# Optimization experiments

Hardware: AMD Instinct MI355X
Metric: run time of the kernel (lower is better)

The kernel has to match this reference:

```python
import jax, jax.numpy as jnp
import numpy as np

N_SAMPLES = 32768
DAMPING = 0.9998
EPS = 1e-8


def sim(home, tensions, masses, gains, mics, forces, home_modifier):
    # forces, home_modifier: (B, M, D, T); home: (1,1,D,1)
    B, M, D, T = forces.shape
    h = home + home_modifier                          # (B,M,D,T)
    f_t = jnp.moveaxis(forces, -1, 0)                 # (T,B,M,D)
    h_t = jnp.moveaxis(h, -1, 0)                      # (T,B,M,D)

    def step(carry, xs):
        pos, vel = carry
        f, hh = xs
        direction = hh - pos
        acc = f + tensions * direction / masses
        vel = (vel + acc) * DAMPING
        pos = pos + vel
        # mic readout: tanh(vel*gains) dotted with mics over dim
        r = jnp.sum(jnp.tanh(vel * gains) * mics, axis=-1)  # (B,M)
        return (pos, vel), (r, direction)

    init = (jnp.zeros((B, M, D), forces.dtype), jnp.zeros((B, M, D), forces.dtype))
    _, (rec, disp) = jax.lax.scan(step, init, (f_t, h_t))
    recording = jnp.moveaxis(rec, 0, -1)              # (B,M,T)
    displacement = jnp.moveaxis(disp, 0, -1)          # (B,M,D,T)
    return recording, displacement


def interpolate_last_axis(x, size):
    # linear interpolation along last axis (F.interpolate mode='linear', align_corners=False)
    T = x.shape[-1]
    pos = jnp.clip((jnp.arange(size) + 0.5) * (T / size) - 0.5, 0.0, T - 1)
    i0 = jnp.floor(pos).astype(jnp.int32)
    i1 = jnp.minimum(i0 + 1, T - 1)
    w = (pos - i0).astype(x.dtype)
    return x[..., i0] * (1 - w) + x[..., i1] * w


def fft_resample(x, desired):
    # zero-pad spectrum to upsample
    spec = jnp.fft.rfft(x, axis=-1, norm='ortho')
    n_coeffs = desired // 2 + 1
    new = jnp.zeros(x.shape[:-1] + (n_coeffs,), dtype=spec.dtype)
    new = new.at[..., :spec.shape[-1]].set(spec)
    return jnp.fft.irfft(new, n=desired, axis=-1, norm='ortho')


def fft_convolve(a, b):
    # linear convolution via 2N-padded FFT, truncated to N
    n = a.shape[-1]
    pa = jnp.pad(a, [(0, 0)] * (a.ndim - 1) + [(0, n)])
    pb = jnp.pad(b, [(0, 0)] * (b.ndim - 1) + [(0, b.shape[-1])])
    spec = jnp.fft.rfft(pa, axis=-1) * jnp.fft.rfft(pb, axis=-1)
    return jnp.fft.irfft(spec, axis=-1)[..., :n]


def forward(forces, home_modifier, filters, home, masses, tensions, gains, mics, to_filter_mixture):
    recording, displacement = sim(home, tensions, masses, gains, mics, forces, home_modifier)
    mixture = jnp.einsum('bmdt,df->bmft', displacement, to_filter_mixture)
    mixture = interpolate_last_axis(mixture, N_SAMPLES)               # (B,M,F,S)
    upsampled = fft_resample(recording, N_SAMPLES)                    # (B,M,S)
    noise = jax.random.uniform(jax.random.key(1), upsampled.shape,
                               dtype=upsampled.dtype, minval=-1.0, maxval=1.0)
    upsampled = jnp.abs(upsampled) * noise
    f = jnp.pad(filters, ((0, 0), (0, 0), (0, N_SAMPLES - filters.shape[-1])))[:, None, :, :]  # (B,1,F,S)
    f = f / (jnp.linalg.norm(f, axis=-1, keepdims=True) + EPS)
    filtered = fft_convolve(f, upsampled[:, :, None, :])              # (B,M,F,S)
    hf = jnp.einsum('bmfs,bmfs->bms', mixture, filtered) + upsampled  # (B,M,S)
    return recording, displacement, hf


def setup_inputs():
    key = jax.random.key(0)
    ks = jax.random.split(key, 8)
    B, M, D, T, F_, L = 2, 32, 64, 2048, 16, 512
    return {
        'forces': jax.random.normal(ks[0], (B, M, D, T), jnp.float32) * 0.01,
        'home_modifier': jax.random.normal(ks[1], (B, M, D, T), jnp.float32),
        'filters': jax.random.normal(ks[2], (B, F_, L), jnp.float32),
        'home': jnp.zeros((1, 1, D, 1), jnp.float32),
        'masses': jax.random.uniform(ks[3], (1, M, 1), jnp.float32, 1000.0, 10000.0),
        'tensions': jax.random.uniform(ks[4], (1, M, D), jnp.float32, 20.0, 30.0),
        'gains': jax.random.uniform(ks[5], (1, M, 1), jnp.float32, 10.0, 100.0),
        'mics': jax.random.uniform(ks[6], (1, M, D), jnp.float32, -1.0, 1.0),
        'to_filter_mixture': jax.random.uniform(ks[7], (D, F_), jnp.float32, -1.0, 1.0),
    }


def reference(forces, home_modifier, filters, home, masses, tensions, gains, mics, to_filter_mixture):
    return forward(forces, home_modifier, filters, home, masses, tensions, gains, mics, to_filter_mixture)
```

## Files before the change

### kernel.cpp

```cpp
#include <hip/hip_runtime.h>
#include <cstdint>
#include <cstddef>

#define DAMP 0.9998f

typedef __attribute__((ext_vector_type(8))) short bf16x8;
typedef __attribute__((ext_vector_type(4))) unsigned short u16x4;
typedef __attribute__((ext_vector_type(4))) float f32x4;

__device__ __forceinline__ unsigned short f2bf(float x) {
    unsigned u = __float_as_uint(x);
    unsigned r = (u + 0x7FFFu + ((u >> 16) & 1u)) >> 16;
    return (unsigned short)r;
}
__device__ __forceinline__ float bf2f(unsigned short v) {
    return __uint_as_float((unsigned)v << 16);
}

__device__ __forceinline__ void threefry_0j(unsigned j, unsigned& o0, unsigned& o1) {
    unsigned x0 = 0u;
    unsigned x1 = j + 1u;
    const unsigned ks2 = 0x1BD11BDBu;
#define TFR(r) { x0 += x1; x1 = (x1 << (r)) | (x1 >> (32 - (r))); x1 ^= x0; }
    TFR(13) TFR(15) TFR(26) TFR(6)
    x0 += 1u;   x1 += ks2 + 1u;
    TFR(17) TFR(29) TFR(16) TFR(24)
    x0 += ks2;  x1 += 0u + 2u;
    TFR(13) TFR(15) TFR(26) TFR(6)
       x1 += 1u + 3u;
    TFR(17) TFR(29) TFR(16) TFR(24)
    x0 += 1u;   x1 += ks2 + 4u;
    TFR(13) TFR(15) TFR(26) TFR(6)
    x0 += ks2;  x1 += 0u + 5u;
#undef TFR
    o0 = x0; o1 = x1;
}

__device__ __forceinline__ float noise_at(unsigned j) {
    unsigned o0, o1;
    threefry_0j(j, o0, o1);
    unsigned bits = o0 ^ o1;
    float u = __uint_as_float((bits >> 9) | 0x3F800000u) - 1.0f;
    return fmaxf(-1.0f, u * 2.0f - 1.0f);
}

__device__ __forceinline__ float dir_val(unsigned u) {
    if (u == 0u) return 2049.f;
    const float PIO = 9.58737992e-05f;
    unsigned y = (2049u * u) & 65535u;
    float sgn = 1.f;
    if (y >= 32768u) { y -= 32768u; sgn = -1.f; }
    unsigned yy = (y > 16384u) ? (32768u - y) : y;
    float sy = sgn * sinf((float)yy * PIO);
    unsigned uu = (u > 16384u) ? (32768u - u) : u;
    float su = sinf((float)uu * PIO);
    return sy / su;
}

__global__ __launch_bounds__(64) void sim_pass1(const float* __restrict__ forces,
                                                const float* __restrict__ hmod,
                                                const float* __restrict__ home,
                                                const float* __restrict__ masses,
                                                const float* __restrict__ tensions,
                                                float* __restrict__ w,
                                                const float* __restrict__ filters,
                                                unsigned short* __restrict__ dirrev,
                                                unsigned short* __restrict__ fnrev) {
    const int blk = blockIdx.x;
    const int d = threadIdx.x;
    if (blk >= 4608) {
        const int row = blk - 4608;
        const float* src = filters + (size_t)row * 512;
        float s = 0.f;
        for (int i = d; i < 512; i += 64) { const float v = src[i]; s += v * v; }
        #pragma unroll
        for (int off = 32; off; off >>= 1) s += __shfl_xor(s, off);
        const float scale = 1.f / (sqrtf(s) + 1e-8f);
        for (int i = d; i < 512; i += 64)
            fnrev[(size_t)row * 512 + i] = f2bf(src[511 - i] * scale);
        return;
    }
    if (blk >= 4096) {
        const unsigned i = (unsigned)(blk - 4096) * 64u + (unsigned)d;
        const unsigned p = i >> 11, k = i & 2047u;
        dirrev[i] = f2bf(dir_val(16u * (2047u - k) + p));
        return;
    }
    const int bm = blk >> 6, c = blk & 63;
    const int m = bm & 31;
    const int t0 = c * 32;
    __shared__ float kv[64];
    __shared__ float hv[64];
    __shared__ __align__(16) float gt[64][33];
    kv[d] = tensions[m * 64 + d] / masses[m];
    hv[d] = home[d];
    __syncthreads();
    for (int i = d; i < 512; i += 64) {
        const int dd = i >> 3, q = (i & 7) * 4;
        const size_t off = ((size_t)bm * 64 + dd) * 2048 + t0 + q;
        const float4 fv = *(const float4*)(forces + off);
        const float4 hm = *(const float4*)(hmod + off);
        const float kk = kv[dd], hh = hv[dd];
        float4 g;
        g.x = fmaf(kk, hh + hm.x, fv.x);
        g.y = fmaf(kk, hh + hm.y, fv.y);
        g.z = fmaf(kk, hh + hm.z, fv.z);
        g.w = fmaf(kk, hh + hm.w, fv.w);
        *(float4*)&gt[dd][q] = g;
    }
    __syncthreads();
    const float k = kv[d];
    float pos = 0.f, vel = 0.f;
    #pragma unroll 8
    for (int ts = 0; ts < 32; ++ts) {
        const float acc = fmaf(-k, pos, gt[d][ts]);
        vel = (vel + acc) * DAMP;
        pos = pos + vel;
    }
    float* wrow = w + (size_t)blk * 128;
    wrow[d] = pos; wrow[64 + d] = vel;
}

__global__ __launch_bounds__(64) void sim_scan(const float* __restrict__ masses,
                                               const float* __restrict__ tensions,
                                               float* __restrict__ w) {
    const int bm = blockIdx.x;
    const int m = bm & 31;
    const int d = threadIdx.x;
    const double kd = (double)(tensions[m * 64 + d] / masses[m]);
    const double cd = (double)DAMP;
    double Ma = 1.0 - cd * kd, Mb = cd, Mc = -cd * kd, Md = cd;
    #pragma unroll
    for (int it = 0; it < 5; ++it) {
        const double na = Ma * Ma + Mb * Mc;
        const double nb = Ma * Mb + Mb * Md;
        const double nc = Mc * Ma + Md * Mc;
        const double nd = Mc * Mb + Md * Md;
        Ma = na; Mb = nb; Mc = nc; Md = nd;
    }
    double pos = 0.0, vel = 0.0;
    float* wb = w + (size_t)bm * 64 * 128;
    for (int c = 0; c < 64; ++c) {
        float* row = wb + c * 128;
        const double wp = (double)row[d];
        const double wv = (double)row[64 + d];
        row[d] = (float)pos;
        row[64 + d] = (float)vel;
        const double np = Ma * pos + Mb * vel + wp;
        const double nv = Mc * pos + Md * vel + wv;
        pos = np; vel = nv;
    }
}

__global__ __launch_bounds__(64) void sim_pass2(const float* __restrict__ forces,
                                                const float* __restrict__ hmod,
                                                const float* __restrict__ home,
                                                const float* __restrict__ masses,
                                                const float* __restrict__ tensions,
                                                const float* __restrict__ gains,
                                                const float* __restrict__ mics,
                                                const float* __restrict__ w,
                                                float* __restrict__ disp,
                                                float* __restrict__ rec) {
    const int blk = blockIdx.x;
    const int bm = blk >> 6, c = blk & 63;
    const int m = bm & 31;
    const int d = threadIdx.x;
    const int t0 = c * 32;
    __shared__ __align__(16) float ft[64][17];
    __shared__ __align__(16) float ht[64][17];
    const float k = tensions[m * 64 + d] / masses[m];
    const float gain = gains[m];
    const float mic = mics[m * 64 + d];
    const float hd = home[d];

    float pos = w[(size_t)blk * 128 + d];
    float vel = w[(size_t)blk * 128 + 64 + d];

    #pragma unroll
    for (int phase = 0; phase < 2; ++phase) {
        const int t0p = t0 + phase * 16;
        for (int i = d; i < 256; i += 64) {
            const int dd = i >> 2, q = (i & 3) * 4;
            const size_t off = ((size_t)bm * 64 + dd) * 2048 + t0p + q;
            *(float4*)&ft[dd][q] = *(const float4*)(forces + off);
            *(float4*)&ht[dd][q] = *(const float4*)(hmod + off);
        }
        __syncthreads();
        #pragma unroll
        for (int ts = 0; ts < 16; ++ts) {
            const float f = ft[d][ts];
            const float h = hd + ht[d][ts];
            const float dir = h - pos;
            const float acc = f + k * dir;
            vel = (vel + acc) * DAMP;
            pos = pos + vel;
            ft[d][ts] = dir;
            const float x = vel * gain;
            const float e = __expf(2.f * x);
            ht[d][ts] = (1.f - 2.f / (e + 1.f)) * mic;
        }
        __syncthreads();
        for (int i = d; i < 256; i += 64) {
            const int dd = i >> 2, q = (i & 3) * 4;
            const size_t off = ((size_t)bm * 64 + dd) * 2048 + t0p + q;
            *(float4*)(disp + off) = *(float4*)&ft[dd][q];
        }
        {
            const int ts = d & 15, part = d >> 4;
            float s = 0.f;
            #pragma unroll
            for (int j = 0; j < 16; ++j) s += ht[16 * part + j][ts];
            s += __shfl_xor(s, 16);
            s += __shfl_xor(s, 32);
            if (d < 16) rec[(size_t)bm * 2048 + t0p + d] = s;
        }
        __syncthreads();
    }
}

__global__ __launch_bounds__(256) void mix_kernel(const float* __restrict__ disp,
                                                  const float* __restrict__ tofm,
                                                  unsigned short* __restrict__ mixture) {
    __shared__ __align__(16) float tf[64][16];
    const int tid = threadIdx.x;
    for (int i = tid; i < 1024; i += 256) tf[i >> 4][i & 15] = tofm[i];
    __syncthreads();
    const int bm = blockIdx.y;
    const int t = blockIdx.x * 256 + tid;
    float acc[16];
    #pragma unroll
    for (int f = 0; f < 16; ++f) acc[f] = 0.f;
    for (int d = 0; d < 64; ++d) {
        const float v = disp[((size_t)bm * 64 + d) * 2048 + t];
        const float4* r4 = (const float4*)tf[d];
        const float4 a4 = r4[0], b4 = r4[1], c4 = r4[2], d4 = r4[3];
        acc[0]  += v * a4.x; acc[1]  += v * a4.y; acc[2]  += v * a4.z; acc[3]  += v * a4.w;
        acc[4]  += v * b4.x; acc[5]  += v * b4.y; acc[6]  += v * b4.z; acc[7]  += v * b4.w;
        acc[8]  += v * c4.x; acc[9]  += v * c4.y; acc[10] += v * c4.z; acc[11] += v * c4.w;
        acc[12] += v * d4.x; acc[13] += v * d4.y; acc[14] += v * d4.z; acc[15] += v * d4.w;
    }
    #pragma unroll
    for (int f = 0; f < 16; ++f)
        mixture[((size_t)bm * 16 + f) * 2048 + t] = f2bf(acc[f]);
}

#define DR_STRIDE 2064u
#define W_STRIDE  5136u
#define W_OFF     33024u
#define RS_SMEM   74112u

__global__ __launch_bounds__(256) void resample_kernel(const float* __restrict__ rec,
                                                       const unsigned short* __restrict__ dirrev,
                                                       unsigned short* __restrict__ upb) {
    const int bm = blockIdx.x;
    const int Q0 = blockIdx.y * 512;
    const int tid = threadIdx.x;
    __shared__ __align__(16) unsigned char smem[RS_SMEM];

    for (int x = tid; x < 2560; x += 256) {
        const int g = (Q0 + x + 1) & 2047;
        const unsigned short bv = f2bf(rec[(size_t)bm * 2048 + g]);
        #pragma unroll
        for (int sg = 0; sg < 8; ++sg) {
            const int y = x - sg;
            if (y >= 0) *(unsigned short*)(smem + W_OFF + sg * W_STRIDE + 2 * y) = bv;
        }
    }

    const int lane = tid & 63;
    const int wv = tid >> 6;
    const int i15 = lane & 15;
    const int g4 = lane >> 4;

    f32x4 acc[8];
    #pragma unroll
    for (int i = 0; i < 8; ++i) acc[i] = (f32x4){0.f, 0.f, 0.f, 0.f};

    const unsigned abase = (unsigned)i15 * DR_STRIDE + 16u * g4;
    const unsigned bbase = W_OFF + (unsigned)(i15 & 7) * W_STRIDE + 16u * (i15 >> 3) + 16u * g4;

    for (int kc = 0; kc < 2; ++kc) {
        if (kc) __syncthreads();
        for (int i = tid; i < 2048; i += 256) {
            const int p = i >> 7, c16 = i & 127;
            *(uint4*)(smem + (unsigned)p * DR_STRIDE + 16u * c16) =
                *(const uint4*)(dirrev + (size_t)p * 2048 + kc * 1024 + 8 * c16);
        }
        __syncthreads();

        for (int kkb = 0; kkb < 4; ++kkb) {
            bf16x8 afr[8];
            #pragma unroll
            for (int kj = 0; kj < 8; ++kj)
                afr[kj] = *(const bf16x8*)(smem + abase + 64u * (kkb * 8 + kj));
            #pragma unroll
            for (int qtl = 0; qtl < 8; ++qtl) {
                const int qt = wv * 8 + qtl;
                const unsigned bb = bbase + 32u * qt + 2048u * kc;
                #pragma unroll
                for (int kj = 0; kj < 8; ++kj) {
                    const bf16x8 bfr = *(const bf16x8*)(smem + bb + 64u * (kkb * 8 + kj));
                    acc[qtl] = __builtin_amdgcn_mfma_f32_16x16x32_bf16(afr[kj], bfr, acc[qtl], 0, 0, 0);
                }
            }
        }
    }

    #pragma unroll
    for (int qtl = 0; qtl < 8; ++qtl) {
        const int qt = wv * 8 + qtl;
        const int q = Q0 + 16 * qt + i15;
        const int sbase = 16 * q + 4 * g4;
        const unsigned jb = (unsigned)bm * 32768u + (unsigned)sbase;
        u16x4 o;
        o[0] = f2bf(fabsf(acc[qtl][0] * (1.f / 8192.f)) * noise_at(jb));
        o[1] = f2bf(fabsf(acc[qtl][1] * (1.f / 8192.f)) * noise_at(jb + 1u));
        o[2] = f2bf(fabsf(acc[qtl][2] * (1.f / 8192.f)) * noise_at(jb + 2u));
        o[3] = f2bf(fabsf(acc[qtl][3] * (1.f / 8192.f)) * noise_at(jb + 3u));
        *(u16x4*)(upb + (size_t)bm * 32768 + sbase) = o;
    }
}

#define W_STR2   3088u
#define MX_OFF   24704u
#define HF_SMEM  26880u

__global__ __launch_bounds__(256) void hf_kernel(const unsigned short* __restrict__ upb,
                                                 const unsigned short* __restrict__ fnrev,
                                                 const unsigned short* __restrict__ mixture,
                                                 float* __restrict__ hf) {
    const int tile = blockIdx.x;
    const int bm = blockIdx.y;
    const int b = bm >> 5;
    const int S0 = tile * 1024;
    const int tbase = tile * 64 - 1;
    const int tid = threadIdx.x;

    __shared__ __align__(16) unsigned char smem[HF_SMEM];
    unsigned short* mixl = (unsigned short*)(smem + MX_OFF);

    for (int x = tid; x < 1536; x += 256) {
        const int gidx = S0 - 511 + x;
        const unsigned short v = (gidx >= 0) ? upb[(size_t)bm * 32768 + gidx]
                                             : (unsigned short)0;
        #pragma unroll
        for (int sg = 0; sg < 8; ++sg) {
            const int y = x - sg;
            if (y >= 0) *(unsigned short*)(smem + sg * W_STR2 + 2 * y) = v;
        }
    }
    for (int i = tid; i < 16 * 66; i += 256) {
        const int f = i / 66, tt = i - f * 66;
        const int t = tbase + tt;
        mixl[f * 68 + tt] = (t >= 0 && t < 2048)
            ? mixture[((size_t)bm * 16 + f) * 2048 + t] : (unsigned short)0;
    }
    const int lane = tid & 63;
    const int i15 = lane & 15;
    const int g4 = lane >> 4;
    const int wv = tid >> 6;
    bf16x8 afr[16];
    #pragma unroll
    for (int kk = 0; kk < 16; ++kk)
        afr[kk] = *(const bf16x8*)(fnrev + (size_t)(b * 16 + i15) * 512 + 32 * kk + 8 * g4);
    __syncthreads();

    for (int rr = 0; rr < 4; ++rr) {
        const int rho = wv * 4 + rr;
        const int sig = rho & 7;
        const unsigned baseR = (unsigned)sig * W_STR2 + 2u * (rho - sig)
                             + 32u * i15 + 16u * g4;
        bf16x8 wfr[16];
        #pragma unroll
        for (int j = 0; j < 8; ++j)
            wfr[j] = *(const bf16x8*)(smem + baseR + 64u * j);
        #pragma unroll
        for (int g = 0; g < 4; ++g) {
            #pragma unroll
            for (int jj = 0; jj < 8; ++jj) {
                const int j = 8 * g + 8 + jj;
                wfr[j & 15] = *(const bf16x8*)(smem + baseR + 64u * (unsigned)j);
            }
            f32x4 acc = {0.f, 0.f, 0.f, 0.f};
            #pragma unroll
            for (int kk = 0; kk < 16; ++kk)
                acc = __builtin_amdgcn_mfma_f32_16x16x32_bf16(afr[kk], wfr[(8 * g + kk) & 15], acc, 0, 0, 0);
            const int s = S0 + 256 * g + rho + 16 * i15;
            float posf = ((float)s + 0.5f) * 0.0625f - 0.5f;
            posf = fminf(fmaxf(posf, 0.f), 2047.f);
            const int i0 = (int)posf;
            const float wg = posf - (float)i0;
            const int i1 = min(i0 + 1, 2047);
            const int t0 = i0 - tbase, t1 = i1 - tbase;
            float part = 0.f;
            #pragma unroll
            for (int r = 0; r < 4; ++r) {
                const int f = 4 * g4 + r;
                const float mv = bf2f(mixl[f * 68 + t0]) * (1.f - wg)
                               + bf2f(mixl[f * 68 + t1]) * wg;
                part += mv * acc[r];
            }
            part += __shfl_xor(part, 16);
            part += __shfl_xor(part, 32);
            if (g4 == 0) {
                const int e = 511 + 256 * g + rho + 16 * i15;
                const float upv = bf2f(*(const unsigned short*)(smem + 2 * e));
                hf[(size_t)bm * 32768 + s] = part + upv;
            }
        }
    }
}

extern "C" void kernel_launch(void* const* d_in, const int* in_sizes, int n_in,
                              void* d_out, int out_size, void* d_ws, size_t ws_size,
                              hipStream_t stream) {
    const float* forces   = (const float*)d_in[0];
    const float* hmod     = (const float*)d_in[1];
    const float* filters  = (const float*)d_in[2];
    const float* home     = (const float*)d_in[3];
    const float* masses   = (const float*)d_in[4];
    const float* tensions = (const float*)d_in[5];
    const float* gains    = (const float*)d_in[6];
    const float* mics     = (const float*)d_in[7];
    const float* tofm     = (const float*)d_in[8];

    float* out  = (float*)d_out;
    float* rec  = out;
    float* disp = out + 131072;
    float* hf   = out + 8519680;

    unsigned short* upb     = (unsigned short*)d_ws;
    unsigned short* mixture = (unsigned short*)((float*)d_ws + 1048576);
    unsigned short* dirrev  = (unsigned short*)((float*)d_ws + 2097152);
    float* w                = (float*)d_ws + 2113536;
    unsigned short* fnrev   = (unsigned short*)((float*)d_ws + 2637824);

    sim_pass1<<<4640, 64, 0, stream>>>(forces, hmod, home, masses, tensions, w,
                                       filters, dirrev, fnrev);
    sim_scan<<<64, 64, 0, stream>>>(masses, tensions, w);
    sim_pass2<<<4096, 64, 0, stream>>>(forces, hmod, home, masses, tensions, gains, mics, w, disp, rec);
    mix_kernel<<<dim3(8, 64), 256, 0, stream>>>(disp, tofm, mixture);
    resample_kernel<<<dim3(64, 4), 256, 0, stream>>>(rec, dirrev, upb);
    hf_kernel<<<dim3(32, 64), 256, 0, stream>>>(upb, fnrev, mixture, hf);
}
```

Before: 120.2 us.

## Merge mix and resample kernels into one launch; split MFMA accumulator chain

```diff
diff --git a/kernel.cpp b/kernel.cpp
--- a/kernel.cpp
+++ b/kernel.cpp
@@ -219,44 +219,48 @@
     }
 }
 
-__global__ __launch_bounds__(256) void mix_kernel(const float* __restrict__ disp,
-                                                  const float* __restrict__ tofm,
-                                                  unsigned short* __restrict__ mixture) {
-    __shared__ __align__(16) float tf[64][16];
-    const int tid = threadIdx.x;
-    for (int i = tid; i < 1024; i += 256) tf[i >> 4][i & 15] = tofm[i];
-    __syncthreads();
-    const int bm = blockIdx.y;
-    const int t = blockIdx.x * 256 + tid;
-    float acc[16];
-    #pragma unroll
-    for (int f = 0; f < 16; ++f) acc[f] = 0.f;
-    for (int d = 0; d < 64; ++d) {
-        const float v = disp[((size_t)bm * 64 + d) * 2048 + t];
-        const float4* r4 = (const float4*)tf[d];
-        const float4 a4 = r4[0], b4 = r4[1], c4 = r4[2], d4 = r4[3];
-        acc[0]  += v * a4.x; acc[1]  += v * a4.y; acc[2]  += v * a4.z; acc[3]  += v * a4.w;
-        acc[4]  += v * b4.x; acc[5]  += v * b4.y; acc[6]  += v * b4.z; acc[7]  += v * b4.w;
-        acc[8]  += v * c4.x; acc[9]  += v * c4.y; acc[10] += v * c4.z; acc[11] += v * c4.w;
-        acc[12] += v * d4.x; acc[13] += v * d4.y; acc[14] += v * d4.z; acc[15] += v * d4.w;
-    }
-    #pragma unroll
-    for (int f = 0; f < 16; ++f)
-        mixture[((size_t)bm * 16 + f) * 2048 + t] = f2bf(acc[f]);
-}
-
 #define DR_STRIDE 2064u
 #define W_STRIDE  5136u
 #define W_OFF     33024u
 #define RS_SMEM   74112u
 
-__global__ __launch_bounds__(256) void resample_kernel(const float* __restrict__ rec,
-                                                       const unsigned short* __restrict__ dirrev,
-                                                       unsigned short* __restrict__ upb) {
-    const int bm = blockIdx.x;
-    const int Q0 = blockIdx.y * 512;
+__global__ __launch_bounds__(256) void mixres_kernel(const float* __restrict__ disp,
+                                                     const float* __restrict__ tofm,
+                                                     unsigned short* __restrict__ mixture,
+                                                     const float* __restrict__ rec,
+                                                     const unsigned short* __restrict__ dirrev,
+                                                     unsigned short* __restrict__ upb) {
+    __shared__ __align__(16) unsigned char smem[RS_SMEM];
     const int tid = threadIdx.x;
-    __shared__ __align__(16) unsigned char smem[RS_SMEM];
+    const int blk = blockIdx.x;
+
+    if (blk < 512) {
+        float* tf = (float*)smem;
+        for (int i = tid; i < 1024; i += 256) tf[i] = tofm[i];
+        __syncthreads();
+        const int bm = blk >> 3;
+        const int t = (blk & 7) * 256 + tid;
+        float acc[16];
+        #pragma unroll
+        for (int f = 0; f < 16; ++f) acc[f] = 0.f;
+        for (int d = 0; d < 64; ++d) {
+            const float v = disp[((size_t)bm * 64 + d) * 2048 + t];
+            const float4* r4 = (const float4*)(tf + d * 16);
+            const float4 a4 = r4[0], b4 = r4[1], c4 = r4[2], d4 = r4[3];
+            acc[0]  += v * a4.x; acc[1]  += v * a4.y; acc[2]  += v * a4.z; acc[3]  += v * a4.w;
+            acc[4]  += v * b4.x; acc[5]  += v * b4.y; acc[6]  += v * b4.z; acc[7]  += v * b4.w;
+            acc[8]  += v * c4.x; acc[9]  += v * c4.y; acc[10] += v * c4.z; acc[11] += v * c4.w;
+            acc[12] += v * d4.x; acc[13] += v * d4.y; acc[14] += v * d4.z; acc[15] += v * d4.w;
+        }
+        #pragma unroll
+        for (int f = 0; f < 16; ++f)
+            mixture[((size_t)bm * 16 + f) * 2048 + t] = f2bf(acc[f]);
+        return;
+    }
+
+    const int rblk = blk - 512;
+    const int bm = rblk >> 2;
+    const int Q0 = (rblk & 3) * 512;
 
     for (int x = tid; x < 2560; x += 256) {
         const int g = (Q0 + x + 1) & 2047;
@@ -382,10 +386,14 @@
                 const int j = 8 * g + 8 + jj;
                 wfr[j & 15] = *(const bf16x8*)(smem + baseR + 64u * (unsigned)j);
             }
-            f32x4 acc = {0.f, 0.f, 0.f, 0.f};
-            #pragma unroll
-            for (int kk = 0; kk < 16; ++kk)
-                acc = __builtin_amdgcn_mfma_f32_16x16x32_bf16(afr[kk], wfr[(8 * g + kk) & 15], acc, 0, 0, 0);
+            f32x4 acc0 = {0.f, 0.f, 0.f, 0.f};
+            f32x4 acc1 = {0.f, 0.f, 0.f, 0.f};
+            #pragma unroll
+            for (int kk = 0; kk < 16; kk += 2) {
+                acc0 = __builtin_amdgcn_mfma_f32_16x16x32_bf16(afr[kk], wfr[(8 * g + kk) & 15], acc0, 0, 0, 0);
+                acc1 = __builtin_amdgcn_mfma_f32_16x16x32_bf16(afr[kk + 1], wfr[(8 * g + kk + 1) & 15], acc1, 0, 0, 0);
+            }
+            const f32x4 acc = acc0 + acc1;
             const int s = S0 + 256 * g + rho + 16 * i15;
             float posf = ((float)s + 0.5f) * 0.0625f - 0.5f;
             posf = fminf(fmaxf(posf, 0.f), 2047.f);
@@ -440,7 +448,6 @@
                                        filters, dirrev, fnrev);
     sim_scan<<<64, 64, 0, stream>>>(masses, tensions, w);
     sim_pass2<<<4096, 64, 0, stream>>>(forces, hmod, home, masses, tensions, gains, mics, w, disp, rec);
-    mix_kernel<<<dim3(8, 64), 256, 0, stream>>>(disp, tofm, mixture);
-    resample_kernel<<<dim3(64, 4), 256, 0, stream>>>(rec, dirrev, upb);
+    mixres_kernel<<<768, 256, 0, stream>>>(disp, tofm, mixture, rec, dirrev, upb);
     hf_kernel<<<dim3(32, 64), 256, 0, stream>>>(upb, fnrev, mixture, hf);
 }
```

Result: slower. 131.5 us (+9.4%).
